# Performance work log

Hardware: AMD Instinct MI355X
Metric: run time of the kernel (lower is better)

The kernel has to match this reference:

```python
import jax, jax.numpy as jnp
import numpy as np
from jax import lax

B, LATENT, HC, COND_OUT, H, INPUT = 64, 512, 1024, 512, 1024, 389
S, SEQ = 16, 512
NOTES = SEQ // S  # 32 notes per subsequence
NL = 2


def _lstm_cell(x, h, c, Wih, Whh, bih, bhh):
    # PyTorch LSTM cell, gate order i, f, g, o
    g = x @ Wih.T + h @ Whh.T + bih + bhh
    i, f, gg, o = jnp.split(g, 4, axis=-1)
    c_new = jax.nn.sigmoid(f) * c + jax.nn.sigmoid(i) * jnp.tanh(gg)
    h_new = jax.nn.sigmoid(o) * jnp.tanh(c_new)
    return h_new, c_new


def setup_inputs() -> dict:
    key = jax.random.key(0)
    ks = iter(jax.random.split(key, 32))
    s = 0.03  # ~ PyTorch LSTM uniform(-1/sqrt(H), 1/sqrt(H)) scale
    def W(shape):
        return jax.random.normal(next(ks), shape, jnp.float32) * s
    return {
        "latent": jax.random.normal(next(ks), (B, LATENT), jnp.float32),
        "target": jax.random.randint(next(ks), (B, SEQ), 0, INPUT),
        "teacher_forcing": 0,
        "h0_dec": jax.random.normal(next(ks), (S, NL, B, H), jnp.float32),
        "c0_dec": jax.random.normal(next(ks), (S, NL, B, H), jnp.float32),
        # conductor LSTM (2 layers)
        "Wih_c0": W((4 * HC, LATENT)), "Whh_c0": W((4 * HC, HC)),
        "bih_c0": W((4 * HC,)), "bhh_c0": W((4 * HC,)),
        "Wih_c1": W((4 * HC, HC)), "Whh_c1": W((4 * HC, HC)),
        "bih_c1": W((4 * HC,)), "bhh_c1": W((4 * HC,)),
        # conductor output projection
        "Wco": W((COND_OUT, HC)), "bco": W((COND_OUT,)),
        # decoder LSTM (2 layers); input = concat(prev_note, emb) -> INPUT+COND_OUT
        "Wih_d0": W((4 * H, INPUT + COND_OUT)), "Whh_d0": W((4 * H, H)),
        "bih_d0": W((4 * H,)), "bhh_d0": W((4 * H,)),
        "Wih_d1": W((4 * H, H)), "Whh_d1": W((4 * H, H)),
        "bih_d1": W((4 * H,)), "bhh_d1": W((4 * H,)),
        # decoder output projection
        "Wdo": W((INPUT, H)), "bdo": W((INPUT,)),
    }


def reference(latent, target, teacher_forcing, h0_dec, c0_dec,
              Wih_c0, Whh_c0, bih_c0, bhh_c0, Wih_c1, Whh_c1, bih_c1, bhh_c1,
              Wco, bco,
              Wih_d0, Whh_d0, bih_d0, bhh_d0, Wih_d1, Whh_d1, bih_d1, bhh_d1,
              Wdo, bdo):
    # use_teacher_forcing is hard-coded False in the source; target is unused.
    del target, teacher_forcing

    def outer(carry, xs):
        hc, cc, prev = carry          # hc, cc: [2,B,HC]; prev: [B,INPUT]
        hd_init, cd_init = xs         # [2,B,H] random decoder init per subsequence
        h0, c0 = _lstm_cell(latent, hc[0], cc[0], Wih_c0, Whh_c0, bih_c0, bhh_c0)
        h1, c1 = _lstm_cell(h0, hc[1], cc[1], Wih_c1, Whh_c1, bih_c1, bhh_c1)
        emb = jnp.tanh(h1 @ Wco.T + bco)  # [B, COND_OUT]

        def inner(ic, _):
            p, hdi, cdi = ic
            x = jnp.concatenate([p, emb], axis=-1)  # [B, INPUT+COND_OUT]
            hd0, cd0 = _lstm_cell(x, hdi[0], cdi[0], Wih_d0, Whh_d0, bih_d0, bhh_d0)
            hd1, cd1 = _lstm_cell(hd0, hdi[1], cdi[1], Wih_d1, Whh_d1, bih_d1, bhh_d1)
            note = jnp.tanh(hd1 @ Wdo.T + bdo)  # [B, INPUT]
            return (note, jnp.stack([hd0, hd1]), jnp.stack([cd0, cd1])), note

        (prev_new, _, _), notes = lax.scan(inner, (prev, hd_init, cd_init), None, length=NOTES)
        return (jnp.stack([h0, h1]), jnp.stack([c0, c1]), prev_new), notes

    init = (jnp.zeros((NL, B, HC), jnp.float32),
            jnp.zeros((NL, B, HC), jnp.float32),
            jnp.zeros((B, INPUT), jnp.float32))
    _, out = lax.scan(outer, init, (h0_dec, c0_dec))
    # out: [S, NOTES, B, INPUT] -> [B, SEQ, INPUT]
    return out.transpose(2, 0, 1, 3).reshape(B, SEQ, INPUT)
```

## Files before the change

### kernel.cpp

```cpp
#include <hip/hip_runtime.h>
#include <hip/hip_bf16.h>

typedef unsigned int  u32;
typedef unsigned short u16;
typedef __attribute__((ext_vector_type(8))) short short8;
typedef __attribute__((ext_vector_type(4))) float f32x4;
typedef __attribute__((ext_vector_type(4))) unsigned int u32x4;
typedef __attribute__((ext_vector_type(2))) unsigned int u32x2;

#define MFMA(a,b,c) __builtin_amdgcn_mfma_f32_16x16x32_bf16(a,b,c,0,0,0)

#define NWG    256
#define KD0    1448
#define KD1    2056
#define KPROJ  1032

#define WS_ARR   0
#define WS_DONE  1024
#define WS_SEM   1536
#define SEM_HD0  0
#define SEM_HD1  1
#define SEM_NOTE 2
#define SEM_I0   3
#define SEM_I1   4

#define NOTE_SZ  26624
#define HD_SZ    65536
#define EMB_S    32768

#define WS_NOTE  4096
#define WS_HD0   (WS_NOTE + 32*NOTE_SZ*2)
#define WS_HD1   (WS_HD0 + 33*HD_SZ*2)
#define WS_HC0   (WS_HD1 + 33*HD_SZ*2)
#define WS_HC1   (WS_HC0 + 2*HD_SZ*2)
#define WS_EMB   (WS_HC1 + 2*HD_SZ*2)
#define WS_LAT   (WS_EMB + 15*EMB_S*2)
#define WS_END   (WS_EMB + 16*EMB_S*2)

#define HC_PAR   65536

#define L_GSC   0
#define L_GC0X  8448
#define L_CC0   12800
#define L_CC1   13824
#define L_BC1   14848
#define L_PACK  14912
#define L_ROLE  16960
#define L_WD0   L_ROLE
#define L_G0E   (L_ROLE + 32*KD0*2)
#define L_CST0  (L_G0E + 8448)
#define L_BD0   (L_CST0 + 2048)
#define L_WPJ   (L_BD0 + 128)
#define L_BPJ   (L_WPJ + 16*KPROJ*2)
#define L_WD1   L_ROLE
#define L_CST1  (L_ROLE + 32*KD1*2)
#define L_BD1   (L_CST1 + 2048)
#define LDS_BYTES 153600

__device__ __forceinline__ u16 f2bf(float f){
  u32 u = __float_as_uint(f);
  u32 r = (u + 0x7FFFu + ((u >> 16) & 1u)) >> 16;
  return (u16)r;
}
__device__ __forceinline__ float sigm(float x){ return 1.f/(1.f + __expf(-x)); }
__device__ __forceinline__ float tanh_(float x){
  float e = __expf(-2.f*fabsf(x));
  float t = (1.f - e)/(1.f + e);
  return x < 0.f ? -t : t;
}
__device__ __forceinline__ short8 ldw8(const float* p0){
  short8 r;
#pragma unroll
  for (int j = 0; j < 8; ++j) r[j] = (short)f2bf(p0[j]);
  return r;
}

__device__ __forceinline__ void gst1(u32* p, u32 v){
  asm volatile("global_store_dword %0, %1, off sc1" :: "v"(p), "v"(v) : "memory");
}
__device__ __forceinline__ void gst4(u16* p, u32x4 v){
  asm volatile("global_store_dwordx4 %0, %1, off sc1" :: "v"(p), "v"(v) : "memory");
}
__device__ __forceinline__ u32 ld1_sc1(const u32* p){
  u32 v;
  asm volatile("global_load_dword %0, %1, off sc1\n\ts_waitcnt vmcnt(0)"
               : "=v"(v) : "v"(p) : "memory");
  return v;
}

#define AISSUE(dst, addr) \
  asm volatile("global_load_dwordx4 %0, %1, off sc1" : "=&v"(dst) : "v"(addr) : "memory")
#define AISSUE_C(dst, addr) \
  asm volatile("global_load_dwordx4 %0, %1, off" : "=&v"(dst) : "v"(addr) : "memory")
#define AWAITN(cnt) do{ \
  asm volatile("s_waitcnt vmcnt(" #cnt ")" ::: "memory"); \
  __builtin_amdgcn_sched_barrier(0x3F7); }while(0)

template<int NA, int NB, bool TWO>
__device__ __forceinline__ void mm_lds(
    const u16* Wl, int ldw16, const u16* xal, const u16* xbl,
    f32x4& a0, f32x4& a1)
{
  constexpr int N = NA + NB;
  constexpr int R = (N < 32) ? N : 32;
  short8 ab[R];
#define XADDR(i) (((i) < NA) ? (xal + (size_t)(i)*2048) : (xbl + (size_t)((i)-NA)*2048))
#define ACONS(i) { \
    a0 = MFMA(ab[(i) % R], *(const short8*)(Wl + (size_t)(i)*32), a0); \
    if constexpr (TWO) a1 = MFMA(ab[(i) % R], *(const short8*)(Wl + ldw16 + (size_t)(i)*32), a1); }
  if constexpr (N <= 32){
#pragma unroll
    for (int i = 0; i < N; ++i) AISSUE_C(ab[i], XADDR(i));
    AWAITN(0);
#pragma unroll
    for (int i = 0; i < N; ++i) ACONS(i);
  } else {
#pragma unroll
    for (int i = 0; i < 32; ++i) AISSUE_C(ab[i], XADDR(i));
#pragma unroll
    for (int i = 0; i < N - 32; ++i){
      AWAITN(31);
      ACONS(i);
      AISSUE_C(ab[i & 31], XADDR(i + 32));
    }
    AWAITN(0);
#pragma unroll
    for (int i = N - 32; i < N; ++i) ACONS(i);
  }
#undef ACONS
#undef XADDR
}

template<int NA, int NB, bool TWO>
__device__ __forceinline__ void mm_gw(
    const float* w00, const float* w01, const float* w10, const float* w11,
    const u16* xal, const u16* xbl, f32x4& a0, f32x4& a1)
{
  constexpr int N = NA + NB;
  static_assert((N % 16) == 0, "");
  short8 ab[16];
#define XADDR(i) (((i) < NA) ? (xal + (size_t)(i)*2048) : (xbl + (size_t)((i)-NA)*2048))
#pragma unroll
  for (int b = 0; b < N/16; ++b){
#pragma unroll
    for (int j = 0; j < 16; ++j) AISSUE(ab[j], XADDR(b*16 + j));
    AWAITN(0);
#pragma unroll
    for (int j = 0; j < 16; ++j){
      const int i = b*16 + j;
      const float* wp0 = (i < NA) ? (w00 + (size_t)i*32) : (w01 + (size_t)(i-NA)*32);
      a0 = MFMA(ab[j], ldw8(wp0), a0);
      if constexpr (TWO){
        const float* wp1 = (i < NA) ? (w10 + (size_t)i*32) : (w11 + (size_t)(i-NA)*32);
        a1 = MFMA(ab[j], ldw8(wp1), a1);
      }
    }
  }
#undef XADDR
}

__device__ __forceinline__ void sem_post_lane(char* ws, int sem, int wg){
  asm volatile("s_waitcnt vmcnt(0)" ::: "memory");
  if (threadIdx.x == 0){
    u32* c = (u32*)(ws + WS_SEM + sem*512 + (wg & 7)*64);
    __hip_atomic_fetch_add(c, 1u, __ATOMIC_RELAXED, __HIP_MEMORY_SCOPE_AGENT);
  }
}
__device__ __forceinline__ void sem_wait(char* ws, int sem, u32 target){
  if (threadIdx.x < 64){
    const int l = threadIdx.x;
    const u32* c = (const u32*)(ws + WS_SEM + sem*512 + l*64);
    for (;;){
      u32 v = (l < 8) ? ld1_sc1(c) : 0u;
#pragma unroll
      for (int off = 32; off; off >>= 1)
        v += (u32)__shfl_xor((int)v, off, 64);
      if (v >= target) break;
      __builtin_amdgcn_s_sleep(1);
    }
  }
  __syncthreads();
}

__device__ __forceinline__ void gbar(char* ws, int grp, int mem, u32 ep){
  u32* arr  = (u32*)(ws + WS_ARR) + grp*32;
  u32* done = (u32*)(ws + WS_DONE);
  asm volatile("s_waitcnt vmcnt(0)" ::: "memory");
  __syncthreads();
  if (threadIdx.x < 64){
    const int l = threadIdx.x;
    if (l == 0) gst1(&arr[mem], ep);
    if (mem == 0){
      for (;;){
        u32 m = (l < 32) ? ld1_sc1(&arr[l]) : ep;
#pragma unroll
        for (int off = 32; off; off >>= 1){
          u32 o = (u32)__shfl_xor((int)m, off, 64);
          m = o < m ? o : m;
        }
        if (m >= ep) break;
      }
      if (l == 0) gst1(&done[grp], ep);
    }
    for (;;){
      u32 m = (l < 8) ? ld1_sc1(&done[l]) : ep;
#pragma unroll
      for (int off = 32; off; off >>= 1){
        u32 o = (u32)__shfl_xor((int)m, off, 64);
        m = o < m ? o : m;
      }
      if (m >= ep) break;
      __builtin_amdgcn_s_sleep(1);
    }
  }
  __syncthreads();
}

struct Params {
  const float *latent, *h0_dec, *c0_dec;
  const float *Wih_c0, *Whh_c0, *bih_c0, *bhh_c0;
  const float *Wih_c1, *Whh_c1, *bih_c1, *bhh_c1;
  const float *Wco, *bco;
  const float *Wih_d0, *Whh_d0, *bih_d0, *bhh_d0;
  const float *Wih_d1, *Whh_d1, *bih_d1, *bhh_d1;
  const float *Wdo, *bdo;
  float* out;
  char* ws;
};

__device__ __forceinline__ void cell_pw(
    const float* g_sc, const float* gadd, const float* bias,
    float* cst, u32* pack, int tid)
{
  const int b = tid & 63, k = tid >> 6;
  u32 hp = 0;
#pragma unroll
  for (int j = 0; j < 2; ++j){
    const int u = 2*k + j;
    float gi = g_sc[b*33 + u];
    float gf = g_sc[b*33 + 8 + u];
    float gg = g_sc[b*33 + 16 + u];
    float go = g_sc[b*33 + 24 + u];
    if (gadd){
      gi += gadd[b*33 + u];      gf += gadd[b*33 + 8 + u];
      gg += gadd[b*33 + 16 + u]; go += gadd[b*33 + 24 + u];
    }
    if (bias){
      gi += bias[u]; gf += bias[8 + u]; gg += bias[16 + u]; go += bias[24 + u];
    }
    float c = sigm(gf)*cst[u*64 + b] + sigm(gi)*tanh_(gg);
    const float h = sigm(go)*tanh_(c);
    cst[u*64 + b] = c;
    hp |= ((u32)f2bf(h)) << (16*j);
  }
  pack[b*4 + k] = hp;
}

__device__ __forceinline__ void cond_pw(
    f32x4 acc, const float* gadd17, const float* bias16,
    float* cstL, u16* pack16, int lane, int wid)
{
  const int r = lane & 15, q = lane >> 4, m0 = wid*16;
  float v[4], vf[4], vg[4], vo[4];
#pragma unroll
  for (int i = 0; i < 4; ++i){
    const int brow = m0 + q*4 + i;
    float x = acc[i];
    if (gadd17) x += gadd17[brow*17 + r];
    if (bias16) x += bias16[r];
    v[i] = x;
  }
#pragma unroll
  for (int i = 0; i < 4; ++i){
    vf[i] = __shfl_xor(v[i], 4, 64);
    vg[i] = __shfl_xor(v[i], 8, 64);
    vo[i] = __shfl_xor(v[i], 12, 64);
  }
  if (r < 4){
#pragma unroll
    for (int i = 0; i < 4; ++i){
      const int brow = m0 + q*4 + i;
      float c = sigm(vf[i])*cstL[r*64 + brow] + sigm(v[i])*tanh_(vg[i]);
      const float h = sigm(vo[i])*tanh_(c);
      cstL[r*64 + brow] = c;
      pack16[brow*4 + r] = f2bf(h);
    }
  }
}

__global__ void init_kernel(const float* latent, char* ws){
  const int i = blockIdx.x*blockDim.x + threadIdx.x;
  if (i < 1024) ((u32*)ws)[i] = 0u;
  if (i < 13312) ((u32*)(ws + WS_NOTE + 31*NOTE_SZ*2))[i] = 0u;
  if (i < 65536){ ((u32*)(ws + WS_HC0))[i] = 0u; ((u32*)(ws + WS_HC1))[i] = 0u; }
  if (i < 32768){
    const int b = i >> 9, k = i & 511;
    ((u16*)(ws + WS_LAT))[((size_t)(k >> 3)*64 + b)*8 + (k & 7)] = f2bf(latent[i]);
  }
}

__global__ void __launch_bounds__(256, 1) decoder_kernel(Params P){
  extern __shared__ char smem[];
  const int wg = blockIdx.x, tid = threadIdx.x;
  const int lane = tid & 63, wid = tid >> 6;
  const int rr = lane & 15, q = lane >> 4, m0 = wid*16;
  const int grp = wg >> 5, mem = wg & 31;

  u16* noteb = (u16*)(P.ws + WS_NOTE);
  u16* hd0R  = (u16*)(P.ws + WS_HD0);
  u16* hd1R  = (u16*)(P.ws + WS_HD1);
  u16* hc0b  = (u16*)(P.ws + WS_HC0);
  u16* hc1b  = (u16*)(P.ws + WS_HC1);
  u16* embA  = (u16*)(P.ws + WS_EMB);
  const u16* latg = (const u16*)(P.ws + WS_LAT);
  u16* hd0_init = hd0R + (size_t)32*HD_SZ;
  u16* hd1_init = hd1R + (size_t)32*HD_SZ;

  float* g_sc  = (float*)(smem + L_GSC);
  float* g_c0x = (float*)(smem + L_GC0X);
  float* cc0   = (float*)(smem + L_CC0);
  float* cc1   = (float*)(smem + L_CC1);
  float* bc1   = (float*)(smem + L_BC1);
  u16*   pack16 = (u16*)(smem + L_PACK);
  u32*   packU32 = (u32*)(smem + L_PACK);
  u16*   Wd0  = (u16*)(smem + L_WD0);
  float* g0e  = (float*)(smem + L_G0E);
  float* cst0 = (float*)(smem + L_CST0);
  float* bd0  = (float*)(smem + L_BD0);
  u16*   Wpj  = (u16*)(smem + L_WPJ);
  float* bpj  = (float*)(smem + L_BPJ);
  u16*   Wd1  = (u16*)(smem + L_WD1);
  float* cst1 = (float*)(smem + L_CST1);
  float* bd1  = (float*)(smem + L_BD1);

  const bool is_d0 = (wg < 128);
  const int lofs = (q*64 + m0 + rr)*8;

  if (is_d0){
    for (int r = wid; r < 32; r += 4){
      const int grow = ((r >> 3) << 10) + 8*wg + (r & 7);
      const float* wih = P.Wih_d0 + (size_t)grow*901;
      const float* whh = P.Whh_d0 + (size_t)grow*1024;
      u16* dst = Wd0 + (size_t)r*KD0;
      for (int c = lane; c < 416; c += 64) dst[c] = (c < 389) ? f2bf(wih[c]) : (u16)0;
      for (int c = lane; c < 1024; c += 64) dst[416 + c] = f2bf(whh[c]);
    }
    if (tid < 32){
      const int grow = ((tid >> 3) << 10) + 8*wg + (tid & 7);
      bd0[tid] = P.bih_d0[grow] + P.bhh_d0[grow];
    }
    if (wg < 25){
      for (int r = wid; r < 16; r += 4){
        const int row = 16*wg + r;
        u16* dst = Wpj + (size_t)r*KPROJ;
        if (row < 389){
          const float* w = P.Wdo + (size_t)row*1024;
          for (int c = lane; c < 1024; c += 64) dst[c] = f2bf(w[c]);
        } else {
          for (int c = lane; c < 1024; c += 64) dst[c] = 0;
        }
      }
      if (tid < 16){
        const int row = 16*wg + tid;
        bpj[tid] = (row < 389) ? P.bdo[row] : 0.f;
      }
    }
  } else {
    const int wl = wg - 128;
    for (int r = wid; r < 32; r += 4){
      const int grow = ((r >> 3) << 10) + 8*wl + (r & 7);
      const float* wih = P.Wih_d1 + (size_t)grow*1024;
      const float* whh = P.Whh_d1 + (size_t)grow*1024;
      u16* dst = Wd1 + (size_t)r*KD1;
      for (int c = lane; c < 1024; c += 64) dst[c] = f2bf(wih[c]);
      for (int c = lane; c < 1024; c += 64) dst[1024 + c] = f2bf(whh[c]);
    }
    if (tid < 32){
      const int grow = ((tid >> 3) << 10) + 8*wl + (tid & 7);
      bd1[tid] = P.bih_d1[grow] + P.bhh_d1[grow];
    }
  }
  if (tid < 256){ cc0[tid] = 0.f; cc1[tid] = 0.f; }
  if (tid < 16){
    const int grow = ((tid >> 2) << 10) + 4*wg + (tid & 3);
    bc1[tid] = P.bih_c1[grow] + P.bhh_c1[grow];
  }
  {
    const int grow = ((rr >> 2) << 10) + 4*wg + (rr & 3);
    f32x4 acc = {0.f,0.f,0.f,0.f}, dummy;
    mm_gw<16,0,false>(P.Wih_c0 + (size_t)grow*512 + q*8, nullptr, nullptr, nullptr,
                      latg + lofs, latg + lofs, acc, dummy);
    const float bias = P.bih_c0[grow] + P.bhh_c0[grow];
#pragma unroll
    for (int i = 0; i < 4; ++i)
      g_c0x[(m0 + q*4 + i)*17 + rr] = acc[i] + bias;
  }
  __syncthreads();

  u32 ep = 0;
#define GBAR() gbar(P.ws, grp, mem, ++ep)

  for (int s = 0; s < 16; ++s){
    const int pc = s & 1;
    const u16* hc0_p = hc0b + (size_t)pc*HC_PAR;
    u16*       hc0_n = hc0b + (size_t)(pc ^ 1)*HC_PAR;
    const u16* hc1_p = hc1b + (size_t)pc*HC_PAR;
    u16*       hc1_n = hc1b + (size_t)(pc ^ 1)*HC_PAR;
    const int grow = ((rr >> 2) << 10) + 4*wg + (rr & 3);

    {
      f32x4 acc = {0.f,0.f,0.f,0.f}, dummy;
      mm_gw<32,0,false>(P.Whh_c0 + (size_t)grow*1024 + q*8, nullptr, nullptr, nullptr,
                        hc0_p + lofs, hc0_p + lofs, acc, dummy);
      cond_pw(acc, g_c0x, nullptr, cc0, pack16, lane, wid);
    }
    __syncthreads();
    if (tid < 64){
      u32x2 v = *(const u32x2*)&packU32[tid*2];
      asm volatile("global_store_dwordx2 %0, %1, off sc1"
                   :: "v"(hc0_n + ((size_t)(wg >> 1)*64 + tid)*8 + (wg & 1)*4), "v"(v) : "memory");
    }
    GBAR();

    {
      f32x4 acc = {0.f,0.f,0.f,0.f}, dummy;
      mm_gw<32,32,false>(P.Wih_c1 + (size_t)grow*1024 + q*8,
                         P.Whh_c1 + (size_t)grow*1024 + q*8, nullptr, nullptr,
                         hc0_n + lofs, hc1_p + lofs, acc, dummy);
      cond_pw(acc, nullptr, bc1, cc1, pack16, lane, wid);
    }
    __syncthreads();
    if (tid < 64){
      u32x2 v = *(const u32x2*)&packU32[tid*2];
      asm volatile("global_store_dwordx2 %0, %1, off sc1"
                   :: "v"(hc1_n + ((size_t)(wg >> 1)*64 + tid)*8 + (wg & 1)*4), "v"(v) : "memory");
    }
    GBAR();

    if (wg < 32){
      const int row = 16*wg + rr;
      f32x4 acc = {0.f,0.f,0.f,0.f}, dummy;
      mm_gw<32,0,false>(P.Wco + (size_t)row*1024 + q*8, nullptr, nullptr, nullptr,
                        hc1_n + lofs, hc1_n + lofs, acc, dummy);
      const float bias = P.bco[row];
#pragma unroll
      for (int i = 0; i < 4; ++i)
        pack16[(m0 + q*4 + i)*16 + rr] = f2bf(tanh_(acc[i] + bias));
      __syncthreads();
      if (tid < 64){
        u16* ea = embA + (size_t)s*EMB_S;
        u32x4 v0 = *(const u32x4*)&packU32[tid*8];
        u32x4 v1 = *(const u32x4*)&packU32[tid*8 + 4];
        gst4(ea + ((size_t)(2*wg)*64 + tid)*8, v0);
        gst4(ea + ((size_t)(2*wg + 1)*64 + tid)*8, v1);
      }
    }
    GBAR();
  }

  for (int s = 0; s < 16; ++s){
    const u32 n0 = (u32)s*32u;
    f32x4 sh0 = {0.f,0.f,0.f,0.f}, sh1 = sh0;
    f32x4 t10 = sh0, t11 = sh0;

    sem_wait(P.ws, SEM_NOTE, 25u*n0);
    __builtin_amdgcn_fence(__ATOMIC_ACQUIRE, "agent");
    __syncthreads();

    if (is_d0){
      {
        const int b = tid & 63, k = tid >> 6;
        const size_t src = ((size_t)(s*2 + 0)*64 + b)*1024 + 8*wg + 2*k;
        cst0[(2*k)*64 + b]     = P.c0_dec[src];
        cst0[(2*k + 1)*64 + b] = P.c0_dec[src + 1];
        packU32[b*4 + k] = (u32)f2bf(P.h0_dec[src]) | ((u32)f2bf(P.h0_dec[src + 1]) << 16);
      }
      __syncthreads();
      if (tid < 64){
        u32x4 v = *(const u32x4*)&packU32[tid*4];
        gst4(hd0_init + ((size_t)wg*64 + tid)*8, v);
        sem_post_lane(P.ws, SEM_I0, wg);
      }
      {
        const int g0 = ((rr >> 3) << 10) + 8*wg + (rr & 7);
        const int g1 = (((rr + 16) >> 3) << 10) + 8*wg + (rr & 7);
        f32x4 a0 = {0.f,0.f,0.f,0.f}, a1 = {0.f,0.f,0.f,0.f};
        const u16* ea = embA + (size_t)s*EMB_S;
        mm_gw<16,0,true>(P.Wih_d0 + (size_t)g0*901 + 389 + q*8, nullptr,
                         P.Wih_d0 + (size_t)g1*901 + 389 + q*8, nullptr,
                         ea + lofs, ea + lofs, a0, a1);
#pragma unroll
        for (int i = 0; i < 4; ++i){
          g0e[(m0 + q*4 + i)*33 + rr]      = a0[i] + bd0[rr];
          g0e[(m0 + q*4 + i)*33 + 16 + rr] = a1[i] + bd0[rr + 16];
        }
      }
      __syncthreads();
    } else {
      const int wl = wg - 128;
      const int b = tid & 63, k = tid >> 6;
      const size_t src = ((size_t)(s*2 + 1)*64 + b)*1024 + 8*wl + 2*k;
      cst1[(2*k)*64 + b]     = P.c0_dec[src];
      cst1[(2*k + 1)*64 + b] = P.c0_dec[src + 1];
      packU32[b*4 + k] = (u32)f2bf(P.h0_dec[src]) | ((u32)f2bf(P.h0_dec[src + 1]) << 16);
      __syncthreads();
      if (tid < 64){
        u32x4 v = *(const u32x4*)&packU32[tid*4];
        gst4(hd1_init + ((size_t)wl*64 + tid)*8, v);
        sem_post_lane(P.ws, SEM_I1, wg);
      }
    }

    for (int t = 0; t < 32; ++t){
      const u32 n = n0 + (u32)t;
      const u16* note_r = noteb + (size_t)((t + 31) & 31)*NOTE_SZ;
      u16*       note_w = noteb + (size_t)t*NOTE_SZ;
      u16* hd0_t = hd0R + (size_t)t*HD_SZ;
      u16* hd1_t = hd1R + (size_t)t*HD_SZ;

      if (is_d0){
        if (t == 0) sem_wait(P.ws, SEM_I0, 128u*(u32)(s + 1));
        else        sem_wait(P.ws, SEM_NOTE, 25u*n);

        f32x4 a0, a1;
        if (t == 0){
          a0 = (f32x4){0.f,0.f,0.f,0.f}; a1 = a0;
          mm_lds<13,32,true>(Wd0 + (size_t)rr*KD0 + q*8, 16*KD0,
                             note_r + lofs, hd0_init + lofs, a0, a1);
        } else {
          a0 = sh0; a1 = sh1;
          mm_lds<13,0,true>(Wd0 + (size_t)rr*KD0 + q*8, 16*KD0,
                            note_r + lofs, note_r + lofs, a0, a1);
        }
#pragma unroll
        for (int i = 0; i < 4; ++i){
          g_sc[(m0 + q*4 + i)*33 + rr]      = a0[i];
          g_sc[(m0 + q*4 + i)*33 + 16 + rr] = a1[i];
        }
        __syncthreads();
        cell_pw(g_sc, g0e, nullptr, cst0, packU32, tid);
        __syncthreads();
        if (tid < 64){
          u32x4 v = *(const u32x4*)&packU32[tid*4];
          gst4(hd0_t + ((size_t)wg*64 + tid)*8, v);
          sem_post_lane(P.ws, SEM_HD0, wg);
        }

        if (t < 31){
          sem_wait(P.ws, SEM_HD0, 128u*(n + 1u));
          sh0 = (f32x4){0.f,0.f,0.f,0.f}; sh1 = sh0;
          mm_lds<32,0,true>(Wd0 + (size_t)rr*KD0 + 416 + q*8, 16*KD0,
                            hd0_t + lofs, hd0_t + lofs, sh0, sh1);
        }

        if (wg < 25){
          sem_wait(P.ws, SEM_HD1, 128u*(n + 1u));
          f32x4 b0 = {0.f,0.f,0.f,0.f}, b1;
          mm_lds<32,0,false>(Wpj + (size_t)rr*KPROJ + q*8, 0,
                             hd1_t + lofs, hd1_t + lofs, b0, b1);
          const int row = 16*wg + rr;
          const int seq = s*32 + t;
          const float bias = bpj[rr];
#pragma unroll
          for (int i = 0; i < 4; ++i){
            const int brow = m0 + q*4 + i;
            const float nv = tanh_(b0[i] + bias);
            if (row < 389) P.out[((size_t)brow*512 + seq)*389 + row] = nv;
            pack16[brow*16 + rr] = f2bf(nv);
          }
          __syncthreads();
          if (tid < 64){
            u32x4 v0 = *(const u32x4*)&packU32[tid*8];
            u32x4 v1 = *(const u32x4*)&packU32[tid*8 + 4];
            gst4(note_w + ((size_t)(2*wg)*64 + tid)*8, v0);
            gst4(note_w + ((size_t)(2*wg + 1)*64 + tid)*8, v1);
            sem_post_lane(P.ws, SEM_NOTE, wg);
          }
        }
      } else {
        sem_wait(P.ws, SEM_HD0, 128u*(n + 1u));
        if (t == 0) sem_wait(P.ws, SEM_I1, 128u*(u32)(s + 1));

        f32x4 a0, a1;
        if (t == 0){
          a0 = (f32x4){0.f,0.f,0.f,0.f}; a1 = a0;
          mm_lds<32,32,true>(Wd1 + (size_t)rr*KD1 + q*8, 16*KD1,
                             hd0_t + lofs, hd1_init + lofs, a0, a1);
        } else {
          a0 = t10; a1 = t11;
          mm_lds<32,0,true>(Wd1 + (size_t)rr*KD1 + q*8, 16*KD1,
                            hd0_t + lofs, hd0_t + lofs, a0, a1);
        }
#pragma unroll
        for (int i = 0; i < 4; ++i){
          g_sc[(m0 + q*4 + i)*33 + rr]      = a0[i];
          g_sc[(m0 + q*4 + i)*33 + 16 + rr] = a1[i];
        }
        __syncthreads();
        cell_pw(g_sc, nullptr, bd1, cst1, packU32, tid);
        __syncthreads();
        if (tid < 64){
          u32x4 v = *(const u32x4*)&packU32[tid*4];
          gst4(hd1_t + ((size_t)(wg - 128)*64 + tid)*8, v);
          sem_post_lane(P.ws, SEM_HD1, wg);
        }

        if (t < 31){
          sem_wait(P.ws, SEM_HD1, 128u*(n + 1u));
          t10 = (f32x4){0.f,0.f,0.f,0.f}; t11 = t10;
          mm_lds<32,0,true>(Wd1 + (size_t)rr*KD1 + 1024 + q*8, 16*KD1,
                            hd1_t + lofs, hd1_t + lofs, t10, t11);
        }
      }
    }
  }
#undef GBAR
}

extern "C" void kernel_launch(void* const* d_in, const int* in_sizes, int n_in,
                              void* d_out, int out_size, void* d_ws, size_t ws_size,
                              hipStream_t stream){
  (void)in_sizes; (void)n_in; (void)out_size;
  if (ws_size < (size_t)WS_END) return;

  Params P;
  P.latent = (const float*)d_in[0];
  P.h0_dec = (const float*)d_in[3];
  P.c0_dec = (const float*)d_in[4];
  P.Wih_c0 = (const float*)d_in[5];  P.Whh_c0 = (const float*)d_in[6];
  P.bih_c0 = (const float*)d_in[7];  P.bhh_c0 = (const float*)d_in[8];
  P.Wih_c1 = (const float*)d_in[9];  P.Whh_c1 = (const float*)d_in[10];
  P.bih_c1 = (const float*)d_in[11]; P.bhh_c1 = (const float*)d_in[12];
  P.Wco    = (const float*)d_in[13]; P.bco    = (const float*)d_in[14];
  P.Wih_d0 = (const float*)d_in[15]; P.Whh_d0 = (const float*)d_in[16];
  P.bih_d0 = (const float*)d_in[17]; P.bhh_d0 = (const float*)d_in[18];
  P.Wih_d1 = (const float*)d_in[19]; P.Whh_d1 = (const float*)d_in[20];
  P.bih_d1 = (const float*)d_in[21]; P.bhh_d1 = (const float*)d_in[22];
  P.Wdo    = (const float*)d_in[23]; P.bdo    = (const float*)d_in[24];
  P.out = (float*)d_out;
  P.ws  = (char*)d_ws;

  hipLaunchKernelGGL(init_kernel, dim3(256), dim3(256), 0, stream,
                     (const float*)d_in[0], (char*)d_ws);

  hipFuncSetAttribute(reinterpret_cast<const void*>(&decoder_kernel),
                      hipFuncAttributeMaxDynamicSharedMemorySize, LDS_BYTES);
  hipLaunchKernelGGL(decoder_kernel, dim3(NWG), dim3(256), LDS_BYTES, stream, P);
}
```

Before: 9.877 ms.

## Compute LSTM pointwise per wave in registers and post semaphores per wave

Drops the LDS round-trip (g_sc scatter, two __syncthreads, shared cell_pw) for the decoder LSTM cell update. Each wave now computes gates from its MFMA accumulators through lane shuffles, keeps the cell state in registers, packs h to bf16 and stores it itself. It then posts its own semaphore increment, so wait targets are scaled by 4. Note output stores move after the semaphore post, and the spin-wait sleep is lengthened. The aim is to cut block-wide barriers on the serial per-step critical path, at the cost of four times more atomics and a longer polling interval.

```diff
diff --git a/kernel.cpp b/kernel.cpp
--- a/kernel.cpp
+++ b/kernel.cpp
@@ -159,6 +159,13 @@
 #undef XADDR
 }
 
+__device__ __forceinline__ void sem_post_wave(char* ws, int sem, int wg){
+  asm volatile("s_waitcnt vmcnt(0)" ::: "memory");
+  if ((threadIdx.x & 63) == 0){
+    u32* c = (u32*)(ws + WS_SEM + sem*512 + (wg & 7)*64);
+    __hip_atomic_fetch_add(c, 1u, __ATOMIC_RELAXED, __HIP_MEMORY_SCOPE_AGENT);
+  }
+}
 __device__ __forceinline__ void sem_post_lane(char* ws, int sem, int wg){
   asm volatile("s_waitcnt vmcnt(0)" ::: "memory");
   if (threadIdx.x == 0){
@@ -176,7 +183,7 @@
       for (int off = 32; off; off >>= 1)
         v += (u32)__shfl_xor((int)v, off, 64);
       if (v >= target) break;
-      __builtin_amdgcn_s_sleep(1);
+      __builtin_amdgcn_s_sleep(4);
     }
   }
   __syncthreads();
@@ -228,34 +235,6 @@
   char* ws;
 };
 
-__device__ __forceinline__ void cell_pw(
-    const float* g_sc, const float* gadd, const float* bias,
-    float* cst, u32* pack, int tid)
-{
-  const int b = tid & 63, k = tid >> 6;
-  u32 hp = 0;
-#pragma unroll
-  for (int j = 0; j < 2; ++j){
-    const int u = 2*k + j;
-    float gi = g_sc[b*33 + u];
-    float gf = g_sc[b*33 + 8 + u];
-    float gg = g_sc[b*33 + 16 + u];
-    float go = g_sc[b*33 + 24 + u];
-    if (gadd){
-      gi += gadd[b*33 + u];      gf += gadd[b*33 + 8 + u];
-      gg += gadd[b*33 + 16 + u]; go += gadd[b*33 + 24 + u];
-    }
-    if (bias){
-      gi += bias[u]; gf += bias[8 + u]; gg += bias[16 + u]; go += bias[24 + u];
-    }
-    float c = sigm(gf)*cst[u*64 + b] + sigm(gi)*tanh_(gg);
-    const float h = sigm(go)*tanh_(c);
-    cst[u*64 + b] = c;
-    hp |= ((u32)f2bf(h)) << (16*j);
-  }
-  pack[b*4 + k] = hp;
-}
-
 __device__ __forceinline__ void cond_pw(
     f32x4 acc, const float* gadd17, const float* bias16,
     float* cstL, u16* pack16, int lane, int wid)
@@ -285,6 +264,44 @@
       cstL[r*64 + brow] = c;
       pack16[brow*4 + r] = f2bf(h);
     }
+  }
+}
+
+__device__ __forceinline__ void pw_store_wave(
+    f32x4 a0, f32x4 a1, float* c4, u32* packU32,
+    u16* dst_base, int wg, int lane, int wid)
+{
+  const int rr = lane & 15, q = lane >> 4, m0 = wid*16;
+  float h[4] = {0.f,0.f,0.f,0.f};
+  f32x4 f_, o_;
+#pragma unroll
+  for (int i = 0; i < 4; ++i){
+    f_[i] = __shfl_xor(a0[i], 8, 64);
+    o_[i] = __shfl_xor(a1[i], 8, 64);
+  }
+  if (rr < 8){
+#pragma unroll
+    for (int i = 0; i < 4; ++i){
+      float c = sigm(f_[i])*c4[i] + sigm(a0[i])*tanh_(a1[i]);
+      c4[i] = c;
+      h[i] = sigm(o_[i])*tanh_(c);
+    }
+  }
+  float h2[4];
+#pragma unroll
+  for (int i = 0; i < 4; ++i) h2[i] = __shfl_xor(h[i], 1, 64);
+  u32* pk = packU32 + wid*64;
+  if (rr < 8 && !(rr & 1)){
+#pragma unroll
+    for (int i = 0; i < 4; ++i){
+      u32 hp = (u32)f2bf(h[i]) | ((u32)f2bf(h2[i]) << 16);
+      pk[(q*4 + i)*4 + (rr >> 1)] = hp;
+    }
+  }
+  asm volatile("s_waitcnt lgkmcnt(0)" ::: "memory");
+  if (lane < 16){
+    u32x4 v = *(const u32x4*)&pk[lane*4];
+    gst4(dst_base + ((size_t)wg*64 + m0 + lane)*8, v);
   }
 }
 
@@ -316,7 +333,6 @@
   u16* hd0_init = hd0R + (size_t)32*HD_SZ;
   u16* hd1_init = hd1R + (size_t)32*HD_SZ;
 
-  float* g_sc  = (float*)(smem + L_GSC);
   float* g_c0x = (float*)(smem + L_GC0X);
   float* cc0   = (float*)(smem + L_CC0);
   float* cc1   = (float*)(smem + L_CC1);
@@ -325,12 +341,10 @@
   u32*   packU32 = (u32*)(smem + L_PACK);
   u16*   Wd0  = (u16*)(smem + L_WD0);
   float* g0e  = (float*)(smem + L_G0E);
-  float* cst0 = (float*)(smem + L_CST0);
   float* bd0  = (float*)(smem + L_BD0);
   u16*   Wpj  = (u16*)(smem + L_WPJ);
   float* bpj  = (float*)(smem + L_BPJ);
   u16*   Wd1  = (u16*)(smem + L_WD1);
-  float* cst1 = (float*)(smem + L_CST1);
   float* bd1  = (float*)(smem + L_BD1);
 
   const bool is_d0 = (wg < 128);
@@ -462,17 +476,22 @@
     const u32 n0 = (u32)s*32u;
     f32x4 sh0 = {0.f,0.f,0.f,0.f}, sh1 = sh0;
     f32x4 t10 = sh0, t11 = sh0;
-
-    sem_wait(P.ws, SEM_NOTE, 25u*n0);
+    float c4[4] = {0.f,0.f,0.f,0.f};
+
+    sem_wait(P.ws, SEM_NOTE, 100u*n0);
     __builtin_amdgcn_fence(__ATOMIC_ACQUIRE, "agent");
     __syncthreads();
 
     if (is_d0){
+      if (rr < 8){
+        const size_t base = ((size_t)(s*2 + 0)*64)*1024 + 8*wg + rr;
+#pragma unroll
+        for (int i = 0; i < 4; ++i)
+          c4[i] = P.c0_dec[base + (size_t)(m0 + q*4 + i)*1024];
+      }
       {
         const int b = tid & 63, k = tid >> 6;
         const size_t src = ((size_t)(s*2 + 0)*64 + b)*1024 + 8*wg + 2*k;
-        cst0[(2*k)*64 + b]     = P.c0_dec[src];
-        cst0[(2*k + 1)*64 + b] = P.c0_dec[src + 1];
         packU32[b*4 + k] = (u32)f2bf(P.h0_dec[src]) | ((u32)f2bf(P.h0_dec[src + 1]) << 16);
       }
       __syncthreads();
@@ -498,11 +517,17 @@
       __syncthreads();
     } else {
       const int wl = wg - 128;
-      const int b = tid & 63, k = tid >> 6;
-      const size_t src = ((size_t)(s*2 + 1)*64 + b)*1024 + 8*wl + 2*k;
-      cst1[(2*k)*64 + b]     = P.c0_dec[src];
-      cst1[(2*k + 1)*64 + b] = P.c0_dec[src + 1];
-      packU32[b*4 + k] = (u32)f2bf(P.h0_dec[src]) | ((u32)f2bf(P.h0_dec[src + 1]) << 16);
+      if (rr < 8){
+        const size_t base = ((size_t)(s*2 + 1)*64)*1024 + 8*wl + rr;
+#pragma unroll
+        for (int i = 0; i < 4; ++i)
+          c4[i] = P.c0_dec[base + (size_t)(m0 + q*4 + i)*1024];
+      }
+      {
+        const int b = tid & 63, k = tid >> 6;
+        const size_t src = ((size_t)(s*2 + 1)*64 + b)*1024 + 8*wl + 2*k;
+        packU32[b*4 + k] = (u32)f2bf(P.h0_dec[src]) | ((u32)f2bf(P.h0_dec[src + 1]) << 16);
+      }
       __syncthreads();
       if (tid < 64){
         u32x4 v = *(const u32x4*)&packU32[tid*4];
@@ -520,7 +545,7 @@
 
       if (is_d0){
         if (t == 0) sem_wait(P.ws, SEM_I0, 128u*(u32)(s + 1));
-        else        sem_wait(P.ws, SEM_NOTE, 25u*n);
+        else        sem_wait(P.ws, SEM_NOTE, 100u*n);
 
         f32x4 a0, a1;
         if (t == 0){
@@ -534,51 +559,56 @@
         }
 #pragma unroll
         for (int i = 0; i < 4; ++i){
-          g_sc[(m0 + q*4 + i)*33 + rr]      = a0[i];
-          g_sc[(m0 + q*4 + i)*33 + 16 + rr] = a1[i];
-        }
-        __syncthreads();
-        cell_pw(g_sc, g0e, nullptr, cst0, packU32, tid);
-        __syncthreads();
-        if (tid < 64){
-          u32x4 v = *(const u32x4*)&packU32[tid*4];
-          gst4(hd0_t + ((size_t)wg*64 + tid)*8, v);
-          sem_post_lane(P.ws, SEM_HD0, wg);
-        }
+          a0[i] += g0e[(m0 + q*4 + i)*33 + rr];
+          a1[i] += g0e[(m0 + q*4 + i)*33 + 16 + rr];
+        }
+        pw_store_wave(a0, a1, c4, packU32, hd0_t, wg, lane, wid);
+        sem_post_wave(P.ws, SEM_HD0, wg);
 
         if (t < 31){
-          sem_wait(P.ws, SEM_HD0, 128u*(n + 1u));
+          sem_wait(P.ws, SEM_HD0, 512u*(n + 1u));
           sh0 = (f32x4){0.f,0.f,0.f,0.f}; sh1 = sh0;
           mm_lds<32,0,true>(Wd0 + (size_t)rr*KD0 + 416 + q*8, 16*KD0,
                             hd0_t + lofs, hd0_t + lofs, sh0, sh1);
         }
 
         if (wg < 25){
-          sem_wait(P.ws, SEM_HD1, 128u*(n + 1u));
+          sem_wait(P.ws, SEM_HD1, 512u*(n + 1u));
           f32x4 b0 = {0.f,0.f,0.f,0.f}, b1;
           mm_lds<32,0,false>(Wpj + (size_t)rr*KPROJ + q*8, 0,
                              hd1_t + lofs, hd1_t + lofs, b0, b1);
           const int row = 16*wg + rr;
-          const int seq = s*32 + t;
           const float bias = bpj[rr];
-#pragma unroll
-          for (int i = 0; i < 4; ++i){
-            const int brow = m0 + q*4 + i;
-            const float nv = tanh_(b0[i] + bias);
-            if (row < 389) P.out[((size_t)brow*512 + seq)*389 + row] = nv;
-            pack16[brow*16 + rr] = f2bf(nv);
+          float nv[4], nv2[4];
+#pragma unroll
+          for (int i = 0; i < 4; ++i) nv[i] = tanh_(b0[i] + bias);
+#pragma unroll
+          for (int i = 0; i < 4; ++i) nv2[i] = __shfl_xor(nv[i], 1, 64);
+          u32* pk = packU32 + wid*128;
+          if (!(rr & 1)){
+            const int g = rr >> 3, pkidx = (rr & 7) >> 1;
+#pragma unroll
+            for (int i = 0; i < 4; ++i){
+              u32 hp = (u32)f2bf(nv[i]) | ((u32)f2bf(nv2[i]) << 16);
+              pk[g*64 + (q*4 + i)*4 + pkidx] = hp;
+            }
           }
-          __syncthreads();
-          if (tid < 64){
-            u32x4 v0 = *(const u32x4*)&packU32[tid*8];
-            u32x4 v1 = *(const u32x4*)&packU32[tid*8 + 4];
-            gst4(note_w + ((size_t)(2*wg)*64 + tid)*8, v0);
-            gst4(note_w + ((size_t)(2*wg + 1)*64 + tid)*8, v1);
-            sem_post_lane(P.ws, SEM_NOTE, wg);
+          asm volatile("s_waitcnt lgkmcnt(0)" ::: "memory");
+          if (lane < 32){
+            const int g = lane >> 4, lr = lane & 15;
+            u32x4 v = *(const u32x4*)&pk[g*64 + lr*4];
+            gst4(note_w + ((size_t)(2*wg + g)*64 + m0 + lr)*8, v);
           }
+          sem_post_wave(P.ws, SEM_NOTE, wg);
+          if (row < 389){
+            const int seq = s*32 + t;
+#pragma unroll
+            for (int i = 0; i < 4; ++i)
+              P.out[((size_t)(m0 + q*4 + i)*512 + seq)*389 + row] = nv[i];
+          }
         }
       } else {
-        sem_wait(P.ws, SEM_HD0, 128u*(n + 1u));
+        sem_wait(P.ws, SEM_HD0, 512u*(n + 1u));
         if (t == 0) sem_wait(P.ws, SEM_I1, 128u*(u32)(s + 1));
 
         f32x4 a0, a1;
@@ -593,20 +623,14 @@
         }
 #pragma unroll
         for (int i = 0; i < 4; ++i){
-          g_sc[(m0 + q*4 + i)*33 + rr]      = a0[i];
-          g_sc[(m0 + q*4 + i)*33 + 16 + rr] = a1[i];
-        }
-        __syncthreads();
-        cell_pw(g_sc, nullptr, bd1, cst1, packU32, tid);
-        __syncthreads();
-        if (tid < 64){
-          u32x4 v = *(const u32x4*)&packU32[tid*4];
-          gst4(hd1_t + ((size_t)(wg - 128)*64 + tid)*8, v);
-          sem_post_lane(P.ws, SEM_HD1, wg);
-        }
+          a0[i] += bd1[rr];
+          a1[i] += bd1[16 + rr];
+        }
+        pw_store_wave(a0, a1, c4, packU32, hd1_t, wg - 128, lane, wid);
+        sem_post_wave(P.ws, SEM_HD1, wg);
 
         if (t < 31){
-          sem_wait(P.ws, SEM_HD1, 128u*(n + 1u));
+          sem_wait(P.ws, SEM_HD1, 512u*(n + 1u));
           t10 = (f32x4){0.f,0.f,0.f,0.f}; t11 = t10;
           mm_lds<32,0,true>(Wd1 + (size_t)rr*KD1 + 1024 + q*8, 16*KD1,
                             hd1_t + lofs, hd1_t + lofs, t10, t11);
```

After: 13.14 ms. 33.0% more time.
